# Performance work log

Hardware: AMD Instinct MI355X
Metric: run time of the kernel (lower is better)

## Reference

```python
import jax, jax.numpy as jnp
import numpy as np

B, S, D, H = 2, 2048, 1024, 16
HD = D // H

def setup_inputs() -> dict:
    key = jax.random.key(0)
    ks = jax.random.split(key, 6)
    X = jax.random.normal(ks[0], (B, S, D), dtype=jnp.float32)
    mask = jax.random.randint(ks[1], (B, 1, S, S), 0, 2, dtype=jnp.int32)
    scale = 1.0 / np.sqrt(D)
    Wq = jax.random.normal(ks[2], (D, D), dtype=jnp.float32) * scale
    Wk = jax.random.normal(ks[3], (D, D), dtype=jnp.float32) * scale
    Wv = jax.random.normal(ks[4], (D, D), dtype=jnp.float32) * scale
    Wo = jax.random.normal(ks[5], (D, D), dtype=jnp.float32) * scale
    return {"X": X, "mask": mask, "Wq": Wq, "Wk": Wk, "Wv": Wv, "Wo": Wo}

def reference(X, mask, Wq, Wk, Wv, Wo):
    b, s, d = X.shape
    # torch nn.Linear(bias=False): y = x @ W.T, W is [out, in]
    def split_heads(Y):
        return Y.reshape(b, s, H, HD).transpose(0, 2, 1, 3)  # [b,h,s,hd]
    Q = split_heads(X @ Wq.T)
    K = split_heads(X @ Wk.T)
    V = split_heads(X @ Wv.T)
    scores = jnp.einsum('bhqd,bhkd->bhqk', Q, K) / jnp.sqrt(jnp.float32(HD))
    # Faithful to original: masked positions filled with -1e-09 (sic)
    scores = jnp.where(mask == 0, jnp.float32(-1e-09), scores)
    # dropout p=0.0 -> identity (applied to scores pre-softmax in original)
    weights = jax.nn.softmax(scores, axis=-1)
    out = jnp.einsum('bhqk,bhkd->bhqd', weights, V)  # [b,h,s,hd]
    out = out.transpose(0, 2, 1, 3).reshape(b, s, d)
    return out @ Wo.T
```

## Files before the change

### kernel.cpp

```cpp
#include <hip/hip_runtime.h>
#include <hip/hip_bf16.h>

using short8  = __attribute__((ext_vector_type(8))) short;
using short4v = __attribute__((ext_vector_type(4))) short;
using f32x4   = __attribute__((ext_vector_type(4))) float;

#if __has_builtin(__builtin_amdgcn_exp2f)
#define EXP2(x) __builtin_amdgcn_exp2f(x)
#else
#define EXP2(x) __expf(0.6931471805599453f*(x))
#endif

__device__ __forceinline__ unsigned short f2bf(float x){
  union { float f; unsigned u; } c; c.f = x;
  unsigned u = c.u + 0x7FFFu + ((c.u >> 16) & 1u);
  return (unsigned short)(u >> 16);
}

__device__ __forceinline__ unsigned pack_bf16_rn(float a, float b){
  __hip_bfloat162 t = __float22bfloat162_rn(make_float2(a, b));
  unsigned u; __builtin_memcpy(&u, &t, 4);
  return u;
}

__global__ __launch_bounds__(256) void prep(const float* __restrict__ X, const int* __restrict__ Mk,
                                            const float* __restrict__ Wq, const float* __restrict__ Wk,
                                            const float* __restrict__ Wv, const float* __restrict__ Wo,
                                            unsigned short* __restrict__ Xb, unsigned short* __restrict__ Wqkv,
                                            unsigned short* __restrict__ Wob, unsigned char* __restrict__ M8)
{
  const int bid = blockIdx.x, tid = threadIdx.x;
  if (bid < 8192){
    const float* src; unsigned short* dst; float scale; int i;
    if (bid < 4096)      { src = X;  dst = Xb;             scale = 1.0f;          i = bid*1024 + tid*4; }
    else if (bid < 5120) { src = Wq; dst = Wqkv;           scale = 0.18033688f;   i = (bid-4096)*1024 + tid*4; }
    else if (bid < 6144) { src = Wk; dst = Wqkv + 1048576; scale = 1.0f;          i = (bid-5120)*1024 + tid*4; }
    else if (bid < 7168) { src = Wv; dst = Wqkv + 2097152; scale = 1.0f;          i = (bid-6144)*1024 + tid*4; }
    else                 { src = Wo; dst = Wob;            scale = 1.0f;          i = (bid-7168)*1024 + tid*4; }
    float4 v = *(const float4*)(src + i);
    ushort4 o;
    o.x = f2bf(v.x * scale); o.y = f2bf(v.y * scale);
    o.z = f2bf(v.z * scale); o.w = f2bf(v.w * scale);
    *(ushort4*)(dst + i) = o;
  } else {
    int i = (bid - 8192)*1024 + tid*4;
    int4 v = *(const int4*)(Mk + i);
    unsigned out = (v.x ? 1u : 0u) | ((v.y ? 1u : 0u) << 8) |
                   ((v.z ? 1u : 0u) << 16) | ((v.w ? 1u : 0u) << 24);
    *(unsigned*)(M8 + i) = out;
  }
}

__device__ __forceinline__ void stage16(const unsigned short* g, unsigned short* l){
  __builtin_amdgcn_global_load_lds(
      (const __attribute__((address_space(1))) void*)g,
      (__attribute__((address_space(3))) void*)l, 16, 0, 0);
}

__global__ __launch_bounds__(256) void gemm_qkv(const unsigned short* __restrict__ A,
                                                const unsigned short* __restrict__ B,
                                                unsigned short* __restrict__ C,
                                                unsigned short* __restrict__ Vg)
{
  __shared__ unsigned short As[128*32];
  __shared__ unsigned short Bs[128*32];
  const int tid = threadIdx.x;
  const int wave = tid >> 6, lane = tid & 63, l16 = lane & 15, quad = lane >> 4;
  const int bm = blockIdx.x * 128, bn = blockIdx.y * 128;
  const int wm = (wave >> 1) * 64, wn = (wave & 1) * 64;
  const int K = 1024;

  f32x4 acc[4][4] = {};
  for (int k0 = 0; k0 < K; k0 += 32){
    #pragma unroll
    for (int c = 0; c < 2; c++){
      int idx = c * 256 + tid;
      int row = idx >> 2, g = (idx & 3) * 8;
      stage16(A + (size_t)(bm + row) * K + k0 + g, &As[idx * 8]);
      stage16(B + (size_t)(bn + row) * K + k0 + g, &Bs[idx * 8]);
    }
    __syncthreads();
    short8 af[4], bf[4];
    #pragma unroll
    for (int i = 0; i < 4; i++) af[i] = *(const short8*)&As[(wm + i*16 + l16)*32 + quad*8];
    #pragma unroll
    for (int j = 0; j < 4; j++) bf[j] = *(const short8*)&Bs[(wn + j*16 + l16)*32 + quad*8];
    #pragma unroll
    for (int i = 0; i < 4; i++)
      #pragma unroll
      for (int j = 0; j < 4; j++)
        acc[i][j] = __builtin_amdgcn_mfma_f32_16x16x32_bf16(af[i], bf[j], acc[i][j], 0, 0, 0);
    __syncthreads();
  }

  if (bn < 2048){
    #pragma unroll
    for (int i = 0; i < 4; i++){
      int mrow = bm + wm + i*16 + quad*4;
      #pragma unroll
      for (int j = 0; j < 4; j++){
        int ncol = bn + wn + j*16 + l16;
        #pragma unroll
        for (int r = 0; r < 4; r++)
          C[(size_t)(mrow + r) * 3072 + ncol] = f2bf(acc[i][j][r]);
      }
    }
  } else {
    #pragma unroll
    for (int i = 0; i < 4; i++){
      int srow = bm + wm + i*16 + quad*4;
      int b = srow >> 11, s = srow & 2047;
      #pragma unroll
      for (int j = 0; j < 4; j++){
        int c = bn - 2048 + wn + j*16 + l16;
        int h = c >> 6, d = c & 63;
        ushort4 o;
        o.x = f2bf(acc[i][j][0]); o.y = f2bf(acc[i][j][1]);
        o.z = f2bf(acc[i][j][2]); o.w = f2bf(acc[i][j][3]);
        *(ushort4*)&Vg[((size_t)(b*16 + h)*64 + d) * 2048 + s] = o;
      }
    }
  }
}

__global__ __launch_bounds__(256) void gemm_out(const unsigned short* __restrict__ A,
                                                const unsigned short* __restrict__ B,
                                                float* __restrict__ Cf)
{
  __shared__ unsigned short As[128*32];
  __shared__ unsigned short Bs[64*32];
  const int tid = threadIdx.x;
  const int wave = tid >> 6, lane = tid & 63, l16 = lane & 15, quad = lane >> 4;
  const int bm = blockIdx.x * 128, bn = blockIdx.y * 64;
  const int wm = (wave >> 1) * 64, wn = (wave & 1) * 32;
  const int K = 1024, N = 1024;

  f32x4 acc[4][2] = {};
  for (int k0 = 0; k0 < K; k0 += 32){
    #pragma unroll
    for (int c = 0; c < 2; c++){
      int idx = c * 256 + tid;
      int row = idx >> 2, g = (idx & 3) * 8;
      stage16(A + (size_t)(bm + row) * K + k0 + g, &As[idx * 8]);
    }
    stage16(B + (size_t)(bn + (tid >> 2)) * K + k0 + (tid & 3) * 8, &Bs[tid * 8]);
    __syncthreads();
    short8 af[4], bf[2];
    #pragma unroll
    for (int i = 0; i < 4; i++) af[i] = *(const short8*)&As[(wm + i*16 + l16)*32 + quad*8];
    #pragma unroll
    for (int j = 0; j < 2; j++) bf[j] = *(const short8*)&Bs[(wn + j*16 + l16)*32 + quad*8];
    #pragma unroll
    for (int i = 0; i < 4; i++)
      #pragma unroll
      for (int j = 0; j < 2; j++)
        acc[i][j] = __builtin_amdgcn_mfma_f32_16x16x32_bf16(af[i], bf[j], acc[i][j], 0, 0, 0);
    __syncthreads();
  }
  #pragma unroll
  for (int i = 0; i < 4; i++){
    int mrow = bm + wm + i*16 + quad*4;
    #pragma unroll
    for (int j = 0; j < 2; j++){
      int ncol = bn + wn + j*16 + l16;
      #pragma unroll
      for (int r = 0; r < 4; r++)
        Cf[(size_t)(mrow + r) * N + ncol] = acc[i][j][r];
    }
  }
}

__global__ __launch_bounds__(256) void attn(const unsigned short* __restrict__ QKV,
                                            const unsigned short* __restrict__ Vg,
                                            const unsigned char* __restrict__ mask8,
                                            unsigned short* __restrict__ O)
{
  __shared__ char smem[33792];
  unsigned short* Ks = (unsigned short*)smem;
  unsigned short* Vt = (unsigned short*)(smem + 16384);
  float* lsums = (float*)(smem + 32768);
  float* red   = (float*)smem;

  const int tid = threadIdx.x, wave = tid >> 6, lane = tid & 63;
  const int l16 = lane & 15, quad = lane >> 4;
  const int id = blockIdx.x;
  const int xcd = id & 7, m = id >> 3;
  const int bh = xcd * 4 + (m >> 5);
  const int qblk = (m & 31) * 64;
  const int b = bh >> 4, h = bh & 15;
  const unsigned short* Qg  = QKV + (size_t)b * 2048 * 3072 + h * 64;
  const unsigned short* Kg  = Qg + 1024;
  const unsigned short* Vgb = Vg + (size_t)bh * 64 * 2048;
  const unsigned char*  mbase = mask8 + (size_t)b * 2048 * 2048;

  short8 qf[4][2];
  #pragma unroll
  for (int nt = 0; nt < 4; nt++)
    #pragma unroll
    for (int ks = 0; ks < 2; ks++)
      qf[nt][ks] = *(const short8*)(Qg + (size_t)(qblk + nt*16 + l16) * 3072 + ks*32 + quad*8);

  f32x4 oacc[4][4] = {};
  float plsum[4] = {0.f, 0.f, 0.f, 0.f};
  const int sw = l16 & 7;

  #pragma unroll
  for (int it = 0; it < 2; it++){
    int s = it * 256 + tid;
    int row = s >> 3, bg = (s & 7) ^ (row & 7);
    stage16(Kg + (size_t)row * 3072 + bg * 8, Ks + s * 8);
    stage16(Vgb + (size_t)row * 2048 + bg * 8, Vt + s * 8);
  }

  for (int c = 0; c < 32; c++){
    const int j0 = c * 64;
    const int buf = (c & 1) * 4096;
    __syncthreads();

    unsigned md[4];
    #pragma unroll
    for (int nt = 0; nt < 4; nt++)
      md[nt] = *(const unsigned*)(mbase + (size_t)(qblk + nt*16 + l16) * 2048 + j0 + wave*16 + quad*4);

    if (c < 31){
      const int nj = j0 + 64, nbuf = ((c + 1) & 1) * 4096;
      #pragma unroll
      for (int it = 0; it < 2; it++){
        int s = it * 256 + tid;
        int row = s >> 3, bg = (s & 7) ^ (row & 7);
        stage16(Kg + (size_t)(nj + row) * 3072 + bg * 8, Ks + nbuf + s * 8);
        stage16(Vgb + (size_t)row * 2048 + nj + bg * 8, Vt + nbuf + s * 8);
      }
    }

    short8 kf0 = *(const short8*)&Ks[buf + (wave*16 + l16) * 64 + ((0 + quad) ^ sw) * 8];
    short8 kf1 = *(const short8*)&Ks[buf + (wave*16 + l16) * 64 + ((4 + quad) ^ sw) * 8];
    short4v b2[4];
    #pragma unroll
    for (int nt = 0; nt < 4; nt++){
      f32x4 a = {0.f, 0.f, 0.f, 0.f};
      a = __builtin_amdgcn_mfma_f32_16x16x32_bf16(kf0, qf[nt][0], a, 0, 0, 0);
      a = __builtin_amdgcn_mfma_f32_16x16x32_bf16(kf1, qf[nt][1], a, 0, 0, 0);
      float p0 = EXP2(a[0] * (float)( md[nt]        & 255u));
      float p1 = EXP2(a[1] * (float)((md[nt] >>  8) & 255u));
      float p2 = EXP2(a[2] * (float)((md[nt] >> 16) & 255u));
      float p3 = EXP2(a[3] * (float)( md[nt] >> 24        ));
      plsum[nt] += (p0 + p1) + (p2 + p3);
      union { unsigned u[2]; short4v s4; } pk;
      pk.u[0] = pack_bf16_rn(p0, p1); pk.u[1] = pack_bf16_rn(p2, p3);
      b2[nt] = pk.s4;
    }

    #pragma unroll
    for (int dt = 0; dt < 4; dt++){
      int physb = (wave*2 + (quad >> 1)) ^ sw;
      short4v a2 = *(const short4v*)&Vt[buf + (dt*16 + l16) * 64 + physb * 8 + (quad & 1) * 4];
      #pragma unroll
      for (int nt = 0; nt < 4; nt++)
        oacc[dt][nt] = __builtin_amdgcn_mfma_f32_16x16x16bf16_1k(a2, b2[nt], oacc[dt][nt], 0, 0, 0);
    }
  }

  float lw[4];
  #pragma unroll
  for (int nt = 0; nt < 4; nt++){
    float v = plsum[nt];
    v += __shfl_xor(v, 16);
    v += __shfl_xor(v, 32);
    lw[nt] = v;
  }
  __syncthreads();
  if (quad == 0){
    #pragma unroll
    for (int nt = 0; nt < 4; nt++) lsums[wave*64 + nt*16 + l16] = lw[nt];
  }
  if (wave == 0){
    #pragma unroll
    for (int dt = 0; dt < 4; dt++)
      #pragma unroll
      for (int nt = 0; nt < 4; nt++)
        *(f32x4*)&red[((dt*4 + nt)*64 + lane)*4] = oacc[dt][nt];
  }
  __syncthreads();
  for (int w = 1; w <= 2; w++){
    if (wave == w){
      #pragma unroll
      for (int dt = 0; dt < 4; dt++)
        #pragma unroll
        for (int nt = 0; nt < 4; nt++){
          f32x4* p = (f32x4*)&red[((dt*4 + nt)*64 + lane)*4];
          *p = *p + oacc[dt][nt];
        }
    }
    __syncthreads();
  }
  if (wave == 3){
    float linv[4];
    #pragma unroll
    for (int nt = 0; nt < 4; nt++){
      int q = nt*16 + l16;
      linv[nt] = 1.0f / (lsums[q] + lsums[64 + q] + lsums[128 + q] + lsums[192 + q]);
    }
    #pragma unroll
    for (int dt = 0; dt < 4; dt++)
      #pragma unroll
      for (int nt = 0; nt < 4; nt++){
        f32x4 t = *(f32x4*)&red[((dt*4 + nt)*64 + lane)*4];
        t = t + oacc[dt][nt];
        unsigned u0 = pack_bf16_rn(t[0] * linv[nt], t[1] * linv[nt]);
        unsigned u1 = pack_bf16_rn(t[2] * linv[nt], t[3] * linv[nt]);
        uint2 st; st.x = u0; st.y = u1;
        *(uint2*)&O[(size_t)(b*2048 + qblk + nt*16 + l16) * 1024 + h*64 + dt*16 + quad*4] = st;
      }
  }
}

extern "C" void kernel_launch(void* const* d_in, const int* in_sizes, int n_in,
                              void* d_out, int out_size, void* d_ws, size_t ws_size,
                              hipStream_t stream)
{
  const float* X  = (const float*)d_in[0];
  const int*   Mk = (const int*)d_in[1];
  const float* Wq = (const float*)d_in[2];
  const float* Wk = (const float*)d_in[3];
  const float* Wv = (const float*)d_in[4];
  const float* Wo = (const float*)d_in[5];
  float* out = (float*)d_out;

  char* ws = (char*)d_ws;
  unsigned short* Xb   = (unsigned short*)(ws + 0);
  unsigned short* Wqkv = (unsigned short*)(ws + 8388608);
  unsigned short* Wob  = (unsigned short*)(ws + 14680064);
  unsigned short* QKV  = (unsigned short*)(ws + 16777216);
  unsigned short* Ob   = (unsigned short*)(ws + 41943040);
  unsigned char*  M8   = (unsigned char*) (ws + 50331648);
  unsigned short* Vg   = (unsigned short*)(ws + 58720256);

  prep<<<16384, 256, 0, stream>>>(X, Mk, Wq, Wk, Wv, Wo, Xb, Wqkv, Wob, M8);
  gemm_qkv<<<dim3(32, 24), 256, 0, stream>>>(Xb, Wqkv, QKV, Vg);
  attn<<<1024, 256, 0, stream>>>(QKV, Vg, M8, Ob);
  gemm_out<<<dim3(32, 16), 256, 0, stream>>>(Ob, Wob, out);
}
```

Baseline: 263.4 us.

## Load K/V fragments directly from global into registers, dropping LDS staging

Removes the shared-memory double buffer for K and V tiles and the per-iteration block barrier. Each wave now reads its own K and V fragments straight from global memory into registers, prefetching the next chunk's K, V and mask while computing the current one. This frees LDS, which may allow more resident blocks, and removes a synchronisation per iteration. In exchange each wave issues its own global loads. Since each wave handles a disjoint 16-key slice of every 64-key chunk, the data is not shared across waves, so L2 and uncoalesced traffic may rise.

```diff
diff --git a/kernel.cpp b/kernel.cpp
--- a/kernel.cpp
+++ b/kernel.cpp
@@ -175,11 +175,9 @@
                                             const unsigned char* __restrict__ mask8,
                                             unsigned short* __restrict__ O)
 {
-  __shared__ char smem[33792];
-  unsigned short* Ks = (unsigned short*)smem;
-  unsigned short* Vt = (unsigned short*)(smem + 16384);
-  float* lsums = (float*)(smem + 32768);
+  __shared__ char smem[17408];
   float* red   = (float*)smem;
+  float* lsums = (float*)(smem + 16384);
 
   const int tid = threadIdx.x, wave = tid >> 6, lane = tid & 63;
   const int l16 = lane & 15, quad = lane >> 4;
@@ -200,47 +198,47 @@
     for (int ks = 0; ks < 2; ks++)
       qf[nt][ks] = *(const short8*)(Qg + (size_t)(qblk + nt*16 + l16) * 3072 + ks*32 + quad*8);
 
+  const unsigned short* kp = Kg + (size_t)(wave*16 + l16) * 3072 + quad*8;
+  const unsigned short* vp = Vgb + (size_t)(l16) * 2048 + wave*16 + quad*4;
+  const unsigned char*  mp = mbase + (size_t)(qblk + l16) * 2048 + wave*16 + quad*4;
+
   f32x4 oacc[4][4] = {};
   float plsum[4] = {0.f, 0.f, 0.f, 0.f};
-  const int sw = l16 & 7;
-
-  #pragma unroll
-  for (int it = 0; it < 2; it++){
-    int s = it * 256 + tid;
-    int row = s >> 3, bg = (s & 7) ^ (row & 7);
-    stage16(Kg + (size_t)row * 3072 + bg * 8, Ks + s * 8);
-    stage16(Vgb + (size_t)row * 2048 + bg * 8, Vt + s * 8);
+
+  short8  kf[2];
+  short4v vf[4];
+  unsigned md[4];
+  {
+    const unsigned short* kr = kp;
+    kf[0] = *(const short8*)(kr);
+    kf[1] = *(const short8*)(kr + 32);
+    #pragma unroll
+    for (int dt = 0; dt < 4; dt++) vf[dt] = *(const short4v*)(vp + dt*16*2048);
+    #pragma unroll
+    for (int nt = 0; nt < 4; nt++) md[nt] = *(const unsigned*)(mp + nt*16*2048);
   }
 
   for (int c = 0; c < 32; c++){
-    const int j0 = c * 64;
-    const int buf = (c & 1) * 4096;
-    __syncthreads();
-
-    unsigned md[4];
-    #pragma unroll
-    for (int nt = 0; nt < 4; nt++)
-      md[nt] = *(const unsigned*)(mbase + (size_t)(qblk + nt*16 + l16) * 2048 + j0 + wave*16 + quad*4);
-
+    const int j0n = (c + 1) * 64;
+    short8  kf_n[2];
+    short4v vf_n[4];
+    unsigned md_n[4];
     if (c < 31){
-      const int nj = j0 + 64, nbuf = ((c + 1) & 1) * 4096;
-      #pragma unroll
-      for (int it = 0; it < 2; it++){
-        int s = it * 256 + tid;
-        int row = s >> 3, bg = (s & 7) ^ (row & 7);
-        stage16(Kg + (size_t)(nj + row) * 3072 + bg * 8, Ks + nbuf + s * 8);
-        stage16(Vgb + (size_t)row * 2048 + nj + bg * 8, Vt + nbuf + s * 8);
-      }
-    }
-
-    short8 kf0 = *(const short8*)&Ks[buf + (wave*16 + l16) * 64 + ((0 + quad) ^ sw) * 8];
-    short8 kf1 = *(const short8*)&Ks[buf + (wave*16 + l16) * 64 + ((4 + quad) ^ sw) * 8];
+      const unsigned short* kr = kp + (size_t)j0n * 3072;
+      kf_n[0] = *(const short8*)(kr);
+      kf_n[1] = *(const short8*)(kr + 32);
+      #pragma unroll
+      for (int dt = 0; dt < 4; dt++) vf_n[dt] = *(const short4v*)(vp + dt*16*2048 + j0n);
+      #pragma unroll
+      for (int nt = 0; nt < 4; nt++) md_n[nt] = *(const unsigned*)(mp + nt*16*2048 + j0n);
+    }
+
     short4v b2[4];
     #pragma unroll
     for (int nt = 0; nt < 4; nt++){
       f32x4 a = {0.f, 0.f, 0.f, 0.f};
-      a = __builtin_amdgcn_mfma_f32_16x16x32_bf16(kf0, qf[nt][0], a, 0, 0, 0);
-      a = __builtin_amdgcn_mfma_f32_16x16x32_bf16(kf1, qf[nt][1], a, 0, 0, 0);
+      a = __builtin_amdgcn_mfma_f32_16x16x32_bf16(kf[0], qf[nt][0], a, 0, 0, 0);
+      a = __builtin_amdgcn_mfma_f32_16x16x32_bf16(kf[1], qf[nt][1], a, 0, 0, 0);
       float p0 = EXP2(a[0] * (float)( md[nt]        & 255u));
       float p1 = EXP2(a[1] * (float)((md[nt] >>  8) & 255u));
       float p2 = EXP2(a[2] * (float)((md[nt] >> 16) & 255u));
@@ -252,13 +250,16 @@
     }
 
     #pragma unroll
-    for (int dt = 0; dt < 4; dt++){
-      int physb = (wave*2 + (quad >> 1)) ^ sw;
-      short4v a2 = *(const short4v*)&Vt[buf + (dt*16 + l16) * 64 + physb * 8 + (quad & 1) * 4];
+    for (int dt = 0; dt < 4; dt++)
       #pragma unroll
       for (int nt = 0; nt < 4; nt++)
-        oacc[dt][nt] = __builtin_amdgcn_mfma_f32_16x16x16bf16_1k(a2, b2[nt], oacc[dt][nt], 0, 0, 0);
-    }
+        oacc[dt][nt] = __builtin_amdgcn_mfma_f32_16x16x16bf16_1k(vf[dt], b2[nt], oacc[dt][nt], 0, 0, 0);
+
+    kf[0] = kf_n[0]; kf[1] = kf_n[1];
+    #pragma unroll
+    for (int dt = 0; dt < 4; dt++) vf[dt] = vf_n[dt];
+    #pragma unroll
+    for (int nt = 0; nt < 4; nt++) md[nt] = md_n[nt];
   }
 
   float lw[4];
```

Result: slower. 317.1 us (+20.4%).

## Software-pipeline attention softmax/PV across chunks and remap GEMM blocks per XCD

Applied to the files above, without the earlier changes.

The attention loop is software-pipelined: each iteration computes the QK^T scores and loads the V fragments and mask for chunk c, while running the exp and PV MFMAs for chunk c-1. A final epilogue handles the last chunk. This is meant to overlap the exp/VALU work with MFMA and LDS latency, at the cost of holding extra live registers for the previous chunk's scores, V fragments and mask. Separately, both GEMMs switch to a 1D grid with an XCD-aware block remap so that blocks on one XCD share B-column tiles, which is meant to improve L2 reuse.

```diff
diff --git a/kernel.cpp b/kernel.cpp
--- a/kernel.cpp
+++ b/kernel.cpp
@@ -66,7 +66,8 @@
   __shared__ unsigned short Bs[128*32];
   const int tid = threadIdx.x;
   const int wave = tid >> 6, lane = tid & 63, l16 = lane & 15, quad = lane >> 4;
-  const int bm = blockIdx.x * 128, bn = blockIdx.y * 128;
+  const int id = blockIdx.x, xcd = id & 7, m = id >> 3;
+  const int bm = (m / 3) * 128, bn = (xcd * 3 + (m % 3)) * 128;
   const int wm = (wave >> 1) * 64, wn = (wave & 1) * 64;
   const int K = 1024;
 
@@ -131,7 +132,8 @@
   __shared__ unsigned short Bs[64*32];
   const int tid = threadIdx.x;
   const int wave = tid >> 6, lane = tid & 63, l16 = lane & 15, quad = lane >> 4;
-  const int bm = blockIdx.x * 128, bn = blockIdx.y * 64;
+  const int id = blockIdx.x, xcd = id & 7, m = id >> 3;
+  const int bm = (m >> 1) * 128, bn = (xcd * 2 + (m & 1)) * 64;
   const int wm = (wave >> 1) * 64, wn = (wave & 1) * 32;
   const int K = 1024, N = 1024;
 
@@ -212,15 +214,14 @@
     stage16(Vgb + (size_t)row * 2048 + bg * 8, Vt + s * 8);
   }
 
+  f32x4   sacc_p[4];
+  short4v vf_p[4];
+  unsigned md_p[4];
+
   for (int c = 0; c < 32; c++){
     const int j0 = c * 64;
     const int buf = (c & 1) * 4096;
     __syncthreads();
-
-    unsigned md[4];
-    #pragma unroll
-    for (int nt = 0; nt < 4; nt++)
-      md[nt] = *(const unsigned*)(mbase + (size_t)(qblk + nt*16 + l16) * 2048 + j0 + wave*16 + quad*4);
 
     if (c < 31){
       const int nj = j0 + 64, nbuf = ((c + 1) & 1) * 4096;
@@ -235,30 +236,70 @@
 
     short8 kf0 = *(const short8*)&Ks[buf + (wave*16 + l16) * 64 + ((0 + quad) ^ sw) * 8];
     short8 kf1 = *(const short8*)&Ks[buf + (wave*16 + l16) * 64 + ((4 + quad) ^ sw) * 8];
-    short4v b2[4];
+    short4v vf_c[4];
+    #pragma unroll
+    for (int dt = 0; dt < 4; dt++){
+      int physb = (wave*2 + (quad >> 1)) ^ sw;
+      vf_c[dt] = *(const short4v*)&Vt[buf + (dt*16 + l16) * 64 + physb * 8 + (quad & 1) * 4];
+    }
+    unsigned md_c[4];
+    #pragma unroll
+    for (int nt = 0; nt < 4; nt++)
+      md_c[nt] = *(const unsigned*)(mbase + (size_t)(qblk + nt*16 + l16) * 2048 + j0 + wave*16 + quad*4);
+
+    f32x4 sacc_c[4];
     #pragma unroll
     for (int nt = 0; nt < 4; nt++){
       f32x4 a = {0.f, 0.f, 0.f, 0.f};
       a = __builtin_amdgcn_mfma_f32_16x16x32_bf16(kf0, qf[nt][0], a, 0, 0, 0);
       a = __builtin_amdgcn_mfma_f32_16x16x32_bf16(kf1, qf[nt][1], a, 0, 0, 0);
-      float p0 = EXP2(a[0] * (float)( md[nt]        & 255u));
-      float p1 = EXP2(a[1] * (float)((md[nt] >>  8) & 255u));
-      float p2 = EXP2(a[2] * (float)((md[nt] >> 16) & 255u));
-      float p3 = EXP2(a[3] * (float)( md[nt] >> 24        ));
+      sacc_c[nt] = a;
+    }
+
+    if (c > 0){
+      short4v b2[4];
+      #pragma unroll
+      for (int nt = 0; nt < 4; nt++){
+        float p0 = EXP2(sacc_p[nt][0] * (float)( md_p[nt]        & 255u));
+        float p1 = EXP2(sacc_p[nt][1] * (float)((md_p[nt] >>  8) & 255u));
+        float p2 = EXP2(sacc_p[nt][2] * (float)((md_p[nt] >> 16) & 255u));
+        float p3 = EXP2(sacc_p[nt][3] * (float)( md_p[nt] >> 24        ));
+        plsum[nt] += (p0 + p1) + (p2 + p3);
+        union { unsigned u[2]; short4v s4; } pk;
+        pk.u[0] = pack_bf16_rn(p0, p1); pk.u[1] = pack_bf16_rn(p2, p3);
+        b2[nt] = pk.s4;
+      }
+      #pragma unroll
+      for (int dt = 0; dt < 4; dt++)
+        #pragma unroll
+        for (int nt = 0; nt < 4; nt++)
+          oacc[dt][nt] = __builtin_amdgcn_mfma_f32_16x16x16bf16_1k(vf_p[dt], b2[nt], oacc[dt][nt], 0, 0, 0);
+    }
+
+    #pragma unroll
+    for (int nt = 0; nt < 4; nt++){ sacc_p[nt] = sacc_c[nt]; md_p[nt] = md_c[nt]; }
+    #pragma unroll
+    for (int dt = 0; dt < 4; dt++) vf_p[dt] = vf_c[dt];
+  }
+
+  {
+    short4v b2[4];
+    #pragma unroll
+    for (int nt = 0; nt < 4; nt++){
+      float p0 = EXP2(sacc_p[nt][0] * (float)( md_p[nt]        & 255u));
+      float p1 = EXP2(sacc_p[nt][1] * (float)((md_p[nt] >>  8) & 255u));
+      float p2 = EXP2(sacc_p[nt][2] * (float)((md_p[nt] >> 16) & 255u));
+      float p3 = EXP2(sacc_p[nt][3] * (float)( md_p[nt] >> 24        ));
       plsum[nt] += (p0 + p1) + (p2 + p3);
       union { unsigned u[2]; short4v s4; } pk;
       pk.u[0] = pack_bf16_rn(p0, p1); pk.u[1] = pack_bf16_rn(p2, p3);
       b2[nt] = pk.s4;
     }
-
-    #pragma unroll
-    for (int dt = 0; dt < 4; dt++){
-      int physb = (wave*2 + (quad >> 1)) ^ sw;
-      short4v a2 = *(const short4v*)&Vt[buf + (dt*16 + l16) * 64 + physb * 8 + (quad & 1) * 4];
+    #pragma unroll
+    for (int dt = 0; dt < 4; dt++)
       #pragma unroll
       for (int nt = 0; nt < 4; nt++)
-        oacc[dt][nt] = __builtin_amdgcn_mfma_f32_16x16x16bf16_1k(a2, b2[nt], oacc[dt][nt], 0, 0, 0);
-    }
+        oacc[dt][nt] = __builtin_amdgcn_mfma_f32_16x16x16bf16_1k(vf_p[dt], b2[nt], oacc[dt][nt], 0, 0, 0);
   }
 
   float lw[4];
@@ -337,7 +378,7 @@
   unsigned short* Vg   = (unsigned short*)(ws + 58720256);
 
   prep<<<16384, 256, 0, stream>>>(X, Mk, Wq, Wk, Wv, Wo, Xb, Wqkv, Wob, M8);
-  gemm_qkv<<<dim3(32, 24), 256, 0, stream>>>(Xb, Wqkv, QKV, Vg);
+  gemm_qkv<<<768, 256, 0, stream>>>(Xb, Wqkv, QKV, Vg);
   attn<<<1024, 256, 0, stream>>>(QKV, Vg, M8, Ob);
-  gemm_out<<<dim3(32, 16), 256, 0, stream>>>(Ob, Wob, out);
-}
+  gemm_out<<<512, 256, 0, stream>>>(Ob, Wob, out);
+}
```

New measurement: 264.6 us. No clear change (+0.4%).

## Split attention PV by output dim via LDS-staged P; XCD-aware GEMM block mapping

Applied to the files above, without the earlier changes.

Previously each wave computed P·V for its own key slice across all output dims, then three serial LDS reduction passes merged the four partial accumulators. Now each wave writes its bf16 P tile to shared memory, a barrier follows, and each wave computes one 16-wide slice of the output dim over all keys. This removes the cross-wave reduction and cuts accumulator registers fourfold, allowing a 3-block occupancy hint. The cost is an extra barrier and LDS traffic every key chunk. Separately, both GEMMs now use a 1D grid remapped so blocks on the same XCD share weight column tiles, for better L2 reuse.

```diff
diff --git a/kernel.cpp b/kernel.cpp
--- a/kernel.cpp
+++ b/kernel.cpp
@@ -66,7 +66,8 @@
   __shared__ unsigned short Bs[128*32];
   const int tid = threadIdx.x;
   const int wave = tid >> 6, lane = tid & 63, l16 = lane & 15, quad = lane >> 4;
-  const int bm = blockIdx.x * 128, bn = blockIdx.y * 128;
+  const int id = blockIdx.x, xcd = id & 7, m = id >> 3;
+  const int bm = (m / 3) * 128, bn = (xcd * 3 + (m % 3)) * 128;
   const int wm = (wave >> 1) * 64, wn = (wave & 1) * 64;
   const int K = 1024;
 
@@ -131,7 +132,8 @@
   __shared__ unsigned short Bs[64*32];
   const int tid = threadIdx.x;
   const int wave = tid >> 6, lane = tid & 63, l16 = lane & 15, quad = lane >> 4;
-  const int bm = blockIdx.x * 128, bn = blockIdx.y * 64;
+  const int id = blockIdx.x, xcd = id & 7, m = id >> 3;
+  const int bm = (m >> 1) * 128, bn = (xcd * 2 + (m & 1)) * 64;
   const int wm = (wave >> 1) * 64, wn = (wave & 1) * 32;
   const int K = 1024, N = 1024;
 
@@ -170,16 +172,16 @@
   }
 }
 
-__global__ __launch_bounds__(256) void attn(const unsigned short* __restrict__ QKV,
-                                            const unsigned short* __restrict__ Vg,
-                                            const unsigned char* __restrict__ mask8,
-                                            unsigned short* __restrict__ O)
-{
-  __shared__ char smem[33792];
+__global__ __launch_bounds__(256, 3) void attn(const unsigned short* __restrict__ QKV,
+                                               const unsigned short* __restrict__ Vg,
+                                               const unsigned char* __restrict__ mask8,
+                                               unsigned short* __restrict__ O)
+{
+  __shared__ char smem[40960];
   unsigned short* Ks = (unsigned short*)smem;
   unsigned short* Vt = (unsigned short*)(smem + 16384);
-  float* lsums = (float*)(smem + 32768);
-  float* red   = (float*)smem;
+  unsigned short* Ps = (unsigned short*)(smem + 32768);
+  float* lsums = (float*)smem;
 
   const int tid = threadIdx.x, wave = tid >> 6, lane = tid & 63;
   const int l16 = lane & 15, quad = lane >> 4;
@@ -200,7 +202,7 @@
     for (int ks = 0; ks < 2; ks++)
       qf[nt][ks] = *(const short8*)(Qg + (size_t)(qblk + nt*16 + l16) * 3072 + ks*32 + quad*8);
 
-  f32x4 oacc[4][4] = {};
+  f32x4 oacc[4] = {};
   float plsum[4] = {0.f, 0.f, 0.f, 0.f};
   const int sw = l16 & 7;
 
@@ -216,11 +218,6 @@
     const int j0 = c * 64;
     const int buf = (c & 1) * 4096;
     __syncthreads();
-
-    unsigned md[4];
-    #pragma unroll
-    for (int nt = 0; nt < 4; nt++)
-      md[nt] = *(const unsigned*)(mbase + (size_t)(qblk + nt*16 + l16) * 2048 + j0 + wave*16 + quad*4);
 
     if (c < 31){
       const int nj = j0 + 64, nbuf = ((c + 1) & 1) * 4096;
@@ -233,9 +230,13 @@
       }
     }
 
+    unsigned md[4];
+    #pragma unroll
+    for (int nt = 0; nt < 4; nt++)
+      md[nt] = *(const unsigned*)(mbase + (size_t)(qblk + nt*16 + l16) * 2048 + j0 + wave*16 + quad*4);
+
     short8 kf0 = *(const short8*)&Ks[buf + (wave*16 + l16) * 64 + ((0 + quad) ^ sw) * 8];
     short8 kf1 = *(const short8*)&Ks[buf + (wave*16 + l16) * 64 + ((4 + quad) ^ sw) * 8];
-    short4v b2[4];
     #pragma unroll
     for (int nt = 0; nt < 4; nt++){
       f32x4 a = {0.f, 0.f, 0.f, 0.f};
@@ -246,18 +247,23 @@
       float p2 = EXP2(a[2] * (float)((md[nt] >> 16) & 255u));
       float p3 = EXP2(a[3] * (float)( md[nt] >> 24        ));
       plsum[nt] += (p0 + p1) + (p2 + p3);
-      union { unsigned u[2]; short4v s4; } pk;
-      pk.u[0] = pack_bf16_rn(p0, p1); pk.u[1] = pack_bf16_rn(p2, p3);
-      b2[nt] = pk.s4;
-    }
-
-    #pragma unroll
-    for (int dt = 0; dt < 4; dt++){
-      int physb = (wave*2 + (quad >> 1)) ^ sw;
-      short4v a2 = *(const short4v*)&Vt[buf + (dt*16 + l16) * 64 + physb * 8 + (quad & 1) * 4];
-      #pragma unroll
-      for (int nt = 0; nt < 4; nt++)
-        oacc[dt][nt] = __builtin_amdgcn_mfma_f32_16x16x16bf16_1k(a2, b2[nt], oacc[dt][nt], 0, 0, 0);
+      uint2 st; st.x = pack_bf16_rn(p0, p1); st.y = pack_bf16_rn(p2, p3);
+      *(uint2*)&Ps[(nt*16 + l16) * 64 + ((wave*2 + (quad >> 1)) ^ sw) * 8 + (quad & 1) * 4] = st;
+    }
+
+    __asm__ volatile("s_waitcnt lgkmcnt(0)" ::: "memory");
+    __builtin_amdgcn_s_barrier();
+    __asm__ volatile("" ::: "memory");
+
+    #pragma unroll
+    for (int kk = 0; kk < 4; kk++){
+      int pb = (kk*2 + (quad >> 1)) ^ sw;
+      short4v a2 = *(const short4v*)&Vt[buf + (wave*16 + l16) * 64 + pb * 8 + (quad & 1) * 4];
+      #pragma unroll
+      for (int nt = 0; nt < 4; nt++){
+        short4v b2 = *(const short4v*)&Ps[(nt*16 + l16) * 64 + pb * 8 + (quad & 1) * 4];
+        oacc[nt] = __builtin_amdgcn_mfma_f32_16x16x16bf16_1k(a2, b2, oacc[nt], 0, 0, 0);
+      }
     }
   }
 
@@ -272,46 +278,22 @@
   __syncthreads();
   if (quad == 0){
     #pragma unroll
-    for (int nt = 0; nt < 4; nt++) lsums[wave*64 + nt*16 + l16] = lw[nt];
-  }
-  if (wave == 0){
-    #pragma unroll
-    for (int dt = 0; dt < 4; dt++)
-      #pragma unroll
-      for (int nt = 0; nt < 4; nt++)
-        *(f32x4*)&red[((dt*4 + nt)*64 + lane)*4] = oacc[dt][nt];
+    for (int nt = 0; nt < 4; nt++) lsums[(nt*16 + l16) * 4 + wave] = lw[nt];
   }
   __syncthreads();
-  for (int w = 1; w <= 2; w++){
-    if (wave == w){
-      #pragma unroll
-      for (int dt = 0; dt < 4; dt++)
-        #pragma unroll
-        for (int nt = 0; nt < 4; nt++){
-          f32x4* p = (f32x4*)&red[((dt*4 + nt)*64 + lane)*4];
-          *p = *p + oacc[dt][nt];
-        }
-    }
-    __syncthreads();
-  }
-  if (wave == 3){
-    float linv[4];
-    #pragma unroll
-    for (int nt = 0; nt < 4; nt++){
-      int q = nt*16 + l16;
-      linv[nt] = 1.0f / (lsums[q] + lsums[64 + q] + lsums[128 + q] + lsums[192 + q]);
-    }
-    #pragma unroll
-    for (int dt = 0; dt < 4; dt++)
-      #pragma unroll
-      for (int nt = 0; nt < 4; nt++){
-        f32x4 t = *(f32x4*)&red[((dt*4 + nt)*64 + lane)*4];
-        t = t + oacc[dt][nt];
-        unsigned u0 = pack_bf16_rn(t[0] * linv[nt], t[1] * linv[nt]);
-        unsigned u1 = pack_bf16_rn(t[2] * linv[nt], t[3] * linv[nt]);
-        uint2 st; st.x = u0; st.y = u1;
-        *(uint2*)&O[(size_t)(b*2048 + qblk + nt*16 + l16) * 1024 + h*64 + dt*16 + quad*4] = st;
-      }
+  float linv[4];
+  #pragma unroll
+  for (int nt = 0; nt < 4; nt++){
+    f32x4 ls = *(const f32x4*)&lsums[(nt*16 + l16) * 4];
+    linv[nt] = 1.0f / (ls[0] + ls[1] + ls[2] + ls[3]);
+  }
+  #pragma unroll
+  for (int nt = 0; nt < 4; nt++){
+    f32x4 t = oacc[nt];
+    unsigned u0 = pack_bf16_rn(t[0] * linv[nt], t[1] * linv[nt]);
+    unsigned u1 = pack_bf16_rn(t[2] * linv[nt], t[3] * linv[nt]);
+    uint2 st; st.x = u0; st.y = u1;
+    *(uint2*)&O[(size_t)(b*2048 + qblk + nt*16 + l16) * 1024 + h*64 + wave*16 + quad*4] = st;
   }
 }
 
@@ -337,7 +319,7 @@
   unsigned short* Vg   = (unsigned short*)(ws + 58720256);
 
   prep<<<16384, 256, 0, stream>>>(X, Mk, Wq, Wk, Wv, Wo, Xb, Wqkv, Wob, M8);
-  gemm_qkv<<<dim3(32, 24), 256, 0, stream>>>(Xb, Wqkv, QKV, Vg);
+  gemm_qkv<<<768, 256, 0, stream>>>(Xb, Wqkv, QKV, Vg);
   attn<<<1024, 256, 0, stream>>>(QKV, Vg, M8, Ob);
-  gemm_out<<<dim3(32, 16), 256, 0, stream>>>(Ob, Wob, out);
-}
+  gemm_out<<<512, 256, 0, stream>>>(Ob, Wob, out);
+}
```

New measurement: 258.9 us. Within noise of the previous version (-1.7%).
